# Performance work log

Measured on AMD Instinct MI355X. Metric: run time of the kernel, lower is better.

Reference implementation:

```python
import jax, jax.numpy as jnp
import numpy as np

B, K, N, T, C = 2, 2, 4096, 8, 3
H = 192            # hidden_dim
NODE_DIM = 10
N_LAYERS = 10
KNN = 16           # k nearest neighbours
TOP_FRAC = 0.4
SHARP = 5.0        # mask_sharpness
S = max(int(TOP_FRAC * N), KNN + 1)   # n_select per graph


def _ln(x, g, b, eps=1e-5):
    mu = x.mean(-1, keepdims=True)
    v = ((x - mu) ** 2).mean(-1, keepdims=True)  # biased var, matches nn.LayerNorm
    return (x - mu) / jnp.sqrt(v + eps) * g + b


def setup_inputs() -> dict:
    key = jax.random.key(0)
    ks = jax.random.split(key, 12)
    rn = lambda k, shape: 0.05 * jax.random.normal(k, shape, jnp.float32)
    F0 = 2 * NODE_DIM + 4   # first EdgeConv MLP in-dim
    FR = 2 * H + 4          # remaining EdgeConv MLP in-dim
    L = N_LAYERS - 1
    return {
        "u_base": jax.random.normal(ks[0], (B, K, N, C), jnp.float32),
        "pos": jax.random.uniform(ks[1], (B, N, 3), dtype=jnp.float32),
        "velocity_in": jax.random.normal(ks[2], (B, T, N, C), jnp.float32),
        "airfoil_mask": (jax.random.uniform(ks[3], (B, N)) < 0.05).astype(jnp.float32),
        "conv0_w1": rn(ks[4], (F0, H)), "conv0_b1": jnp.zeros((H,)),
        "conv0_w2": rn(ks[5], (H, H)), "conv0_b2": jnp.zeros((H,)),
        "conv0_g": jnp.ones((H,)), "conv0_be": jnp.zeros((H,)),
        "convs_w1": rn(ks[6], (L, FR, H)), "convs_b1": jnp.zeros((L, H)),
        "convs_w2": rn(ks[7], (L, H, H)), "convs_b2": jnp.zeros((L, H)),
        "convs_g": jnp.ones((L, H)), "convs_be": jnp.zeros((L, H)),
        "head_g": jnp.ones((H,)), "head_be": jnp.zeros((H,)),
        "head_w1": rn(ks[8], (H, H)), "head_b1": jnp.zeros((H,)),
        "head_w2": rn(ks[9], (H, 3)), "head_b2": jnp.zeros((3,)),
    }


def reference(u_base, pos, velocity_in, airfoil_mask,
              conv0_w1, conv0_b1, conv0_w2, conv0_b2, conv0_g, conv0_be,
              convs_w1, convs_b1, convs_w2, convs_b2, convs_g, convs_be,
              head_g, head_be, head_w1, head_b1, head_w2, head_b2):
    # --- variance gating (torch .var/.std are unbiased) ---
    var_pp = jnp.var(velocity_in, axis=1, ddof=1).sum(-1)                      # [B,N]
    var_z = (var_pp - var_pp.mean(1, keepdims=True)) / (
        jnp.std(var_pp, axis=1, ddof=1, keepdims=True) + 1e-8)
    soft_mask = jax.nn.sigmoid(SHARP * var_z) * (1.0 - airfoil_mask)           # [B,N]

    # --- select top-variance points per graph ---
    _, top_idx = jax.lax.top_k(var_pp, S)                                      # [B,S]
    pos_sel = jnp.take_along_axis(pos, top_idx[..., None], axis=1)             # [B,S,3]
    mask_sel = jnp.take_along_axis(soft_mask, top_idx, axis=1)[..., None]      # [B,S,1]
    v_last = velocity_in[:, -1]                                                # [B,N,C]
    ub_sel = jnp.take_along_axis(u_base, top_idx[:, None, :, None], axis=2)    # [B,K,S,C]
    vl_sel = jnp.take_along_axis(v_last, top_idx[..., None], axis=1)           # [B,S,C]
    vf_sel = jnp.take_along_axis(var_pp[..., None], top_idx[..., None], axis=1)
    static = jnp.concatenate([vl_sel, pos_sel, vf_sel], -1)                    # [B,S,7]
    x0 = jnp.concatenate(
        [ub_sel, jnp.broadcast_to(static[:, None], (B, K, S, 7))], -1)         # [B,K,S,10]

    def per_graph(x, pos_b):  # x: [K,S,F0], pos_b: [S,3]
        # kNN graph (self excluded via +inf diagonal, as in the chunked cdist)
        d2 = jnp.sum((pos_b[:, None] - pos_b[None]) ** 2, -1)                  # [S,S]
        d2 = d2.at[jnp.arange(S), jnp.arange(S)].set(jnp.inf)
        _, knn = jax.lax.top_k(-d2, KNN)                                       # [S,KNN]
        # PyG convention with edge_index=stack([targets, sources]):
        # i = edge_index[1] = knn neighbours, j = edge_index[0] = centre nodes
        idx_i = knn.reshape(-1)                     # [E] aggregation targets
        idx_j = jnp.repeat(jnp.arange(S), KNN)      # [E]
        rel = pos_b[idx_i] - pos_b[idx_j]           # pos[edge_index[1]] - pos[edge_index[0]]
        dist = jnp.linalg.norm(rel, axis=-1, keepdims=True)
        ea = jnp.concatenate([rel, dist], -1)       # [E,4]
        ea_b = jnp.broadcast_to(ea, (K,) + ea.shape)

        def conv(h, w1, b1, w2, b2, g, be):
            hi = h[:, idx_i]
            hj = h[:, idx_j]
            m = jnp.concatenate([hi, hj - hi, ea_b], -1)                       # [K,E,2F+4]
            m = jax.nn.gelu(m @ w1 + b1, approximate=False) @ w2 + b2          # [K,E,H]
            agg = jnp.zeros((K, S, H), h.dtype).at[:, idx_i].add(m)
            return _ln(agg, g, be)

        h = conv(x, conv0_w1, conv0_b1, conv0_w2, conv0_b2, conv0_g, conv0_be)
        for l in range(N_LAYERS - 1):
            h = conv(h, convs_w1[l], convs_b1[l], convs_w2[l], convs_b2[l],
                     convs_g[l], convs_be[l]) + h
        hh = _ln(h, head_g, head_be)
        return jax.nn.gelu(hh @ head_w1 + head_b1, approximate=False) @ head_w2 + head_b2

    delta = jax.vmap(per_graph)(x0, pos_sel)        # [B,K,S,3]
    delta = delta * mask_sel[:, None]               # [B,1,S,1]

    def scatter_b(idx, d):  # idx [S], d [K,S,3]
        return jnp.zeros((K, N, C), d.dtype).at[:, idx].set(d)

    delta_full = jax.vmap(scatter_b)(top_idx, delta)            # [B,K,N,C]
    return (u_base + delta_full) * (1.0 - airfoil_mask)[:, None, :, None]
```

## Files before the change

### kernel.cpp

```cpp
#include <hip/hip_runtime.h>
#include <hip/hip_bf16.h>
#include <math.h>

#define B_ 2
#define K_ 2
#define NN_ 4096
#define T_ 8
#define C_ 3
#define H_ 192
#define S_ 1638
#define KK_ 16
#define E_ (S_*KK_)
#define NROW (B_*K_*S_)
#define SHARP_ 5.0f

typedef __hip_bfloat16 bf;
typedef unsigned long long ull;
typedef __bf16 bf16x8 __attribute__((ext_vector_type(8)));
typedef float f32x4 __attribute__((ext_vector_type(4)));

__device__ int   g_isbf16;
__device__ __align__(16) float g_var[B_*NN_];
__device__ __align__(16) float g_vs1[B_*16];
__device__ __align__(16) float g_vs2[B_*16];
__device__ __align__(16) int   g_topidx[B_*S_];
__device__ __align__(16) float g_possel[B_*S_*3];
__device__ __align__(16) float g_masksel[B_*S_];
__device__ __align__(16) float g_x0[NROW*10];
__device__ __align__(16) int   g_knn[B_*E_];
__device__ __align__(16) float g_ea[B_*E_*4];
__device__ __align__(16) int   g_indeg[B_*S_];
__device__ __align__(16) int   g_cursor[B_*S_];
__device__ __align__(16) int   g_off[B_*(S_+1)];
__device__ __align__(16) int   g_list[B_*E_];
__device__ __align__(16) float g_P[(size_t)NROW*H_];
__device__ __align__(16) bf    g_Qbf[(size_t)NROW*H_];
__device__ __align__(16) float g_h[(size_t)NROW*H_];
__device__ __align__(16) bf    g_abf[(size_t)NROW*H_];
__device__ __align__(16) bf    g_w2p[(size_t)11*H_*H_];
__device__ __align__(16) bf    g_wcp[(size_t)9*H_*384];

__device__ __forceinline__ float bf2f(bf x){ return __bfloat162float(x); }
__device__ __forceinline__ float LD(const void* p, long i){
  return g_isbf16 ? __bfloat162float(((const bf*)p)[i]) : ((const float*)p)[i];
}
__device__ __forceinline__ float LDi(const void* p, long i, int isb){
  return isb ? __bfloat162float(((const bf*)p)[i]) : ((const float*)p)[i];
}
__device__ __forceinline__ float gelu_f(float x){
  float ax = fabsf(x)*0.70710678118654752f;
  float t = 1.0f/(1.0f + 0.3275911f*ax);
  float p = t*(0.254829592f + t*(-0.284496736f + t*(1.421413741f + t*(-1.453152027f + t*1.061405429f))));
  float er = 1.0f - p*__expf(-ax*ax);
  er = copysignf(er, x);
  return 0.5f*x*(1.0f + er);
}

__global__ __launch_bounds__(256) void k_var(const void* __restrict__ vel,
                                             const void* __restrict__ ub,
                                             const void* __restrict__ pos){
  __shared__ int s_bad;
  int b = blockIdx.y;
  int bx = blockIdx.x;
  int tid = threadIdx.x;
  if (tid == 0) s_bad = 0;
  __syncthreads();
  {
    const bf* pa = (const bf*)ub; const bf* pb = (const bf*)pos; const bf* pc = (const bf*)vel;
    int bad = 0;
    #pragma unroll
    for (int s = 0; s < 2; ++s){
      float va = __bfloat162float(pa[tid + s*256]);
      float vb = __bfloat162float(pb[tid + s*256]);
      float vc = __bfloat162float(pc[tid + s*256]);
      if (!(fabsf(va) <= 1000.f)) bad = 1;
      if (!(fabsf(vb) <= 1000.f)) bad = 1;
      if (!(fabsf(vc) <= 1000.f)) bad = 1;
    }
    if (bad) atomicOr(&s_bad, 1);
  }
  __syncthreads();
  int isb = (s_bad == 0) ? 1 : 0;
  if (bx == 0 && b == 0 && tid == 0) g_isbf16 = isb;
  int zi = (b*16 + bx)*256 + tid;
  if (zi < B_*S_){ g_indeg[zi] = 0; g_cursor[zi] = 0; }
  int n = bx*256 + tid;
  float v = 0.f;
  #pragma unroll
  for (int c = 0; c < 3; ++c){
    float x[8];
    #pragma unroll
    for (int t = 0; t < 8; ++t)
      x[t] = LDi(vel, ((long)(b*T_+t)*NN_ + n)*3 + c, isb);
    float m = __fadd_rn(__fadd_rn(__fadd_rn(x[0],x[1]), __fadd_rn(x[2],x[3])),
                        __fadd_rn(__fadd_rn(x[4],x[5]), __fadd_rn(x[6],x[7]))) / 8.0f;
    float d[8];
    #pragma unroll
    for (int t = 0; t < 8; ++t){ float dd = __fadd_rn(x[t], -m); d[t] = __fmul_rn(dd,dd); }
    float sv = __fadd_rn(__fadd_rn(__fadd_rn(d[0],d[1]), __fadd_rn(d[2],d[3])),
                         __fadd_rn(__fadd_rn(d[4],d[5]), __fadd_rn(d[6],d[7])));
    v = __fadd_rn(v, sv / 7.0f);
  }
  g_var[b*NN_ + n] = v;
  float s1 = v, s2 = v*v;
  #pragma unroll
  for (int o = 32; o; o >>= 1){ s1 += __shfl_xor(s1,o,64); s2 += __shfl_xor(s2,o,64); }
  __shared__ float r1[4], r2[4];
  int lane = tid & 63, wid = tid >> 6;
  if (!lane){ r1[wid]=s1; r2[wid]=s2; }
  __syncthreads();
  if (tid == 0){
    g_vs1[b*16 + bx] = r1[0]+r1[1]+r1[2]+r1[3];
    g_vs2[b*16 + bx] = r2[0]+r2[1]+r2[2]+r2[3];
  }
}

__global__ __launch_bounds__(256) void k_rank(const void* __restrict__ pos){
  int b = blockIdx.y;
  int i = blockIdx.x*4 + (threadIdx.x >> 6);
  int lane = threadIdx.x & 63;
  float vi = g_var[b*NN_+i];
  int rank = 0;
  for (int j = lane; j < NN_; j += 64){
    float vj = g_var[b*NN_+j];
    rank += ((vj > vi) || (vj == vi && j < i)) ? 1 : 0;
  }
  #pragma unroll
  for (int o = 32; o; o >>= 1) rank += __shfl_xor(rank, o, 64);
  if (lane == 0 && rank < S_){
    g_topidx[b*S_ + rank] = i;
    long gi = (long)(b*S_ + rank)*3;
    g_possel[gi+0] = LD(pos, ((long)b*NN_+i)*3+0);
    g_possel[gi+1] = LD(pos, ((long)b*NN_+i)*3+1);
    g_possel[gi+2] = LD(pos, ((long)b*NN_+i)*3+2);
  }
}

#define GATH_BLKS 7
__global__ __launch_bounds__(256) void k_knngather(const void* __restrict__ pos,
                                                   const void* __restrict__ ub,
                                                   const void* __restrict__ vel,
                                                   const void* __restrict__ air){
  int b = blockIdx.y;
  int bx = blockIdx.x;
  if (bx < GATH_BLKS){
    int s = bx*256 + threadIdx.x;
    if (s >= S_) return;
    int gi = b*S_ + s;
    int node = g_topidx[gi];
    float px = g_possel[(long)gi*3+0];
    float py = g_possel[(long)gi*3+1];
    float pz = g_possel[(long)gi*3+2];
    float S1 = 0.f, S2 = 0.f;
    #pragma unroll
    for (int t = 0; t < 16; ++t){ S1 += g_vs1[b*16+t]; S2 += g_vs2[b*16+t]; }
    float mean = S1*(1.f/NN_);
    float sd = sqrtf(fmaxf((S2 - S1*S1*(1.f/NN_))*(1.f/(NN_-1)), 0.f));
    float vf = g_var[b*NN_+node];
    float z = (vf-mean)/(sd+1e-8f);
    float sig = 1.f/(1.f+expf(-SHARP_*z));
    g_masksel[gi] = sig*(1.f - LD(air, b*NN_+node));
    float vl0 = LD(vel, ((long)(b*T_+7)*NN_+node)*3+0);
    float vl1 = LD(vel, ((long)(b*T_+7)*NN_+node)*3+1);
    float vl2 = LD(vel, ((long)(b*T_+7)*NN_+node)*3+2);
    for (int k = 0; k < K_; ++k){
      long row = (long)(b*K_+k)*S_ + s;
      float* x = g_x0 + row*10;
      x[0]=LD(ub, ((long)(b*K_+k)*NN_+node)*3+0);
      x[1]=LD(ub, ((long)(b*K_+k)*NN_+node)*3+1);
      x[2]=LD(ub, ((long)(b*K_+k)*NN_+node)*3+2);
      x[3]=vl0; x[4]=vl1; x[5]=vl2;
      x[6]=px;  x[7]=py;  x[8]=pz;
      x[9]=vf;
    }
    return;
  }
  __shared__ float px[S_], py[S_], pz[S_];
  int j = (bx - GATH_BLKS)*4 + (threadIdx.x >> 6);
  int lane = threadIdx.x & 63;
  for (int t = threadIdx.x; t < S_; t += 256){
    long gi = (long)(b*S_ + t)*3;
    px[t] = g_possel[gi+0];
    py[t] = g_possel[gi+1];
    pz[t] = g_possel[gi+2];
  }
  __syncthreads();
  if (j >= S_) return;
  float xj=px[j], yj=py[j], zj=pz[j];
  float dist[KK_]; int id[KK_];
  #pragma unroll
  for (int t = 0; t < KK_; ++t){ dist[t]=3.0e38f; id[t]=0x7fffffff; }
  for (int c = lane; c < S_; c += 64){
    if (c == j) continue;
    float dx=__fadd_rn(px[c],-xj), dy=__fadd_rn(py[c],-yj), dz=__fadd_rn(pz[c],-zj);
    float d2 = __fadd_rn(__fadd_rn(__fmul_rn(dx,dx), __fmul_rn(dy,dy)), __fmul_rn(dz,dz));
    if (d2 < dist[KK_-1]){
      int p = 0;
      #pragma unroll
      for (int q = 0; q < KK_; ++q) p += (dist[q] <= d2) ? 1 : 0;
      #pragma unroll
      for (int q = KK_-1; q >= 1; --q){
        bool mv = (q > p);
        dist[q] = mv ? dist[q-1] : dist[q];
        id[q]   = mv ? id[q-1]   : id[q];
      }
      #pragma unroll
      for (int q = 0; q < KK_; ++q){ if (q == p){ dist[q] = d2; id[q] = c; } }
    }
  }
  unsigned selid = 0;
  #pragma unroll
  for (int t = 0; t < KK_; ++t){
    float mv = dist[0];
    #pragma unroll
    for (int o = 32; o; o >>= 1) mv = fminf(mv, __shfl_xor(mv, o, 64));
    unsigned cand = (dist[0] == mv) ? (unsigned)id[0] : 0xFFFFFFFFu;
    #pragma unroll
    for (int o = 32; o; o >>= 1){
      unsigned other = (unsigned)__shfl_xor((int)cand, o, 64);
      cand = (cand < other) ? cand : other;
    }
    if (dist[0] == mv && (unsigned)id[0] == cand){
      #pragma unroll
      for (int q = 0; q < KK_-1; ++q){ dist[q]=dist[q+1]; id[q]=id[q+1]; }
      dist[KK_-1] = 3.0e38f; id[KK_-1] = 0x7fffffff;
    }
    if (lane == t) selid = cand;
  }
  if (lane < KK_){
    int i = (int)selid;
    g_knn[(b*S_+j)*KK_ + lane] = i;
    float rx = __fadd_rn(px[i],-xj), ry = __fadd_rn(py[i],-yj), rz = __fadd_rn(pz[i],-zj);
    float dd = sqrtf(__fadd_rn(__fadd_rn(__fmul_rn(rx,rx), __fmul_rn(ry,ry)), __fmul_rn(rz,rz)));
    float* o = g_ea + ((long)b*E_ + j*KK_ + lane)*4;
    o[0]=rx; o[1]=ry; o[2]=rz; o[3]=dd;
    atomicAdd(&g_indeg[b*S_+i], 1);
  }
}

__global__ void k_scan(){
  __shared__ int sA[2048], sB[2048];
  int b = blockIdx.x, tid = threadIdx.x;
  for (int i = tid; i < 2048; i += 1024) sA[i] = (i < S_) ? g_indeg[b*S_+i] : 0;
  __syncthreads();
  int *src = sA, *dst = sB;
  for (int d = 1; d < 2048; d <<= 1){
    for (int i = tid; i < 2048; i += 1024) dst[i] = src[i] + (i >= d ? src[i-d] : 0);
    __syncthreads();
    int* t2 = src; src = dst; dst = t2;
  }
  if (tid == 0) g_off[b*(S_+1)] = 0;
  for (int i = tid; i < S_; i += 1024) g_off[b*(S_+1)+i+1] = src[i];
}

#define PW2_BLKS 1584
#define PWC_BLKS 2592
#define INIT_BLKS 192
#define FILL_BLKS 205
#define PROJ_BLKS 410
__global__ void k_packall(const void* __restrict__ c0w2, const void* __restrict__ cw2,
                          const void* __restrict__ hw1, const void* __restrict__ cw1,
                          const void* __restrict__ ub, const void* __restrict__ air,
                          float* __restrict__ out, const void* __restrict__ c0w1){
  int blk = blockIdx.x;
  if (blk < PW2_BLKS){
    int gi = blk*256 + threadIdx.x;
    if (gi >= 11*H_*H_) return;
    int mat = gi / (H_*H_), r = gi - mat*(H_*H_);
    int k = r / H_, n = r - (r/H_)*H_;
    float v;
    if (mat == 0)      v = LD(c0w2, (long)k*H_ + n);
    else if (mat <= 9) v = LD(cw2, (long)(mat-1)*H_*H_ + (long)k*H_ + n);
    else               v = LD(hw1, (long)k*H_ + n);
    int t = k>>5, q = (k>>3)&3, jj = k&7;
    g_w2p[(size_t)mat*H_*H_ + (((t*4+q)*H_ + n)*8 + jj)] = __float2bfloat16(v);
  } else if (blk < PW2_BLKS + PWC_BLKS){
    int gi = (blk - PW2_BLKS)*256 + threadIdx.x;
    if (gi >= 9*H_*384) return;
    int l = gi / (H_*384), r = gi - l*(H_*384);
    int k = r / 384, n = r - (r/384)*384;
    long base = (long)l*388*H_;
    float v;
    if (n < H_) v = LD(cw1, base + (long)k*H_ + n) - LD(cw1, base + (long)(H_+k)*H_ + n);
    else        v = LD(cw1, base + (long)(H_+k)*H_ + (n-H_));
    int t = k>>5, q = (k>>3)&3, jj = k&7;
    g_wcp[(size_t)l*(H_*384) + (((t*4+q)*384 + n)*8 + jj)] = __float2bfloat16(v);
  } else if (blk < PW2_BLKS + PWC_BLKS + INIT_BLKS){
    int gi = (blk - PW2_BLKS - PWC_BLKS)*256 + threadIdx.x;
    int n = (gi/3) % NN_;
    int b = gi / (K_*NN_*C_);
    float a = 1.f - LD(air, b*NN_+n);
    out[gi] = LD(ub, gi) * a;
  } else if (blk < PW2_BLKS + PWC_BLKS + INIT_BLKS + FILL_BLKS){
    int idx = (blk - PW2_BLKS - PWC_BLKS - INIT_BLKS)*256 + threadIdx.x;
    if (idx >= B_*E_) return;
    int b = idx / E_, e = idx - b*E_;
    int i = g_knn[idx];
    int slot = atomicAdd(&g_cursor[b*S_+i], 1);
    g_list[b*E_ + g_off[b*(S_+1)+i] + slot] = e;
  } else {
    __shared__ float xs[16][10];
    __shared__ float wP[10][192];
    __shared__ float wQ[10][192];
    int tid = threadIdx.x;
    long rowBase = (long)(blk - PW2_BLKS - PWC_BLKS - INIT_BLKS - FILL_BLKS) * 16;
    for (int idx = tid; idx < 1920; idx += 256){
      int f = idx / 192, n = idx - (idx/192)*192;
      float a = LD(c0w1, f*H_+n), b = LD(c0w1, (10+f)*H_+n);
      wP[f][n] = a - b; wQ[f][n] = b;
    }
    for (int idx = tid; idx < 160; idx += 256){
      int r = idx / 10, f = idx - (idx/10)*10;
      long row = rowBase + r; if (row >= NROW) row = NROW-1;
      xs[r][f] = g_x0[row*10 + f];
    }
    __syncthreads();
    for (int o = tid; o < 16*384; o += 256){
      int r = o / 384, n = o - (o/384)*384;
      long row = rowBase + r;
      if (row >= NROW) continue;
      float acc = 0.f;
      if (n < 192){
        #pragma unroll
        for (int f = 0; f < 10; ++f) acc += xs[r][f]*wP[f][n];
        g_P[row*192 + n] = acc;
      } else {
        int nc = n - 192;
        #pragma unroll
        for (int f = 0; f < 10; ++f) acc += xs[r][f]*wQ[f][nc];
        g_Qbf[row*192 + nc] = __float2bfloat16(acc);
      }
    }
  }
}

__global__ __launch_bounds__(192) void k_aggedge(const void* __restrict__ w1cB, long w1cO,
                                                 const void* __restrict__ b1B, long b1O){
  int o = blockIdx.x;
  int t = o & 7, s = o >> 3;
  int bk = t >> 1;
  int row = bk*S_ + 2*s + (t & 1);
  int col = threadIdx.x;
  int i = row - bk*S_, b = bk >> 1;
  int off = g_off[b*(S_+1)+i];
  int deg = g_off[b*(S_+1)+i+1] - off;
  float w0 = LD(w1cB, w1cO+col),       w1v = LD(w1cB, w1cO+H_+col);
  float w2v = LD(w1cB, w1cO+2*H_+col), w3v = LD(w1cB, w1cO+3*H_+col);
  float base = g_P[(size_t)row*H_ + col] + LD(b1B, b1O+col);
  const int* lst = g_list + b*E_ + off;
  const bf* Q = g_Qbf + (size_t)bk*S_*H_;
  const float* EA = g_ea + (size_t)b*E_*4;
  float acc = 0.f;
  int d = 0;
  for (; d + 8 <= deg; d += 8){
    int e[8];
    #pragma unroll
    for (int u = 0; u < 8; ++u) e[u] = lst[d+u];
    float4 a[8];
    #pragma unroll
    for (int u = 0; u < 8; ++u) a[u] = *reinterpret_cast<const float4*>(EA + (size_t)e[u]*4);
    float qv[8];
    #pragma unroll
    for (int u = 0; u < 8; ++u) qv[u] = bf2f(Q[(size_t)(e[u]>>4)*H_ + col]);
    #pragma unroll
    for (int u = 0; u < 8; ++u)
      acc += gelu_f(base + qv[u] + a[u].x*w0 + a[u].y*w1v + a[u].z*w2v + a[u].w*w3v);
  }
  for (; d + 4 <= deg; d += 4){
    int e0 = lst[d], e1 = lst[d+1], e2 = lst[d+2], e3 = lst[d+3];
    float4 a0 = *reinterpret_cast<const float4*>(EA + (size_t)e0*4);
    float4 a1 = *reinterpret_cast<const float4*>(EA + (size_t)e1*4);
    float4 a2 = *reinterpret_cast<const float4*>(EA + (size_t)e2*4);
    float4 a3 = *reinterpret_cast<const float4*>(EA + (size_t)e3*4);
    float q0 = bf2f(Q[(size_t)(e0>>4)*H_ + col]);
    float q1 = bf2f(Q[(size_t)(e1>>4)*H_ + col]);
    float q2 = bf2f(Q[(size_t)(e2>>4)*H_ + col]);
    float q3 = bf2f(Q[(size_t)(e3>>4)*H_ + col]);
    acc += gelu_f(base + q0 + a0.x*w0 + a0.y*w1v + a0.z*w2v + a0.w*w3v);
    acc += gelu_f(base + q1 + a1.x*w0 + a1.y*w1v + a1.z*w2v + a1.w*w3v);
    acc += gelu_f(base + q2 + a2.x*w0 + a2.y*w1v + a2.z*w2v + a2.w*w3v);
    acc += gelu_f(base + q3 + a3.x*w0 + a3.y*w1v + a3.z*w2v + a3.w*w3v);
  }
  for (; d < deg; ++d){
    int e = lst[d];
    float4 a = *reinterpret_cast<const float4*>(EA + (size_t)e*4);
    float qv = bf2f(Q[(size_t)(e>>4)*H_ + col]);
    acc += gelu_f(base + qv + a.x*w0 + a.y*w1v + a.z*w2v + a.w*w3v);
  }
  g_abf[(size_t)row*H_ + col] = __float2bfloat16(acc);
}

template<int RES, int DOPQ, int DOHEAD>
__global__ __launch_bounds__(512) void k_lnpq(const void* __restrict__ biasB, long biasO,
                                              const void* __restrict__ gB, long gO,
                                              const void* __restrict__ beB, long beO,
                                              int bOff, int pqOff,
                                              const void* __restrict__ hg, const void* __restrict__ hbe,
                                              const void* __restrict__ hb1, const void* __restrict__ hw2,
                                              const void* __restrict__ hb2, const void* __restrict__ ubase,
                                              const void* __restrict__ air, float* __restrict__ out,
                                              int M){
  const bf* A  = g_abf;
  const bf* Bp = g_w2p + bOff;
  int tid = threadIdx.x;
  int wv = tid >> 6, lane = tid & 63;
  int q = lane >> 4, l16 = lane & 15;
  long rowBase = (long)blockIdx.x * 16;
  __shared__ float tile[16][200];
  __shared__ bf    ybf[16][200];
  __shared__ float srow[16], rrow[16];
  {
    f32x4 acc[2];
    acc[0] = (f32x4){0.f,0.f,0.f,0.f};
    acc[1] = (f32x4){0.f,0.f,0.f,0.f};
    #pragma unroll
    for (int t = 0; t < 6; ++t){
      int kof = t*32 + q*8;
      long r = rowBase + l16; if (r >= M) r = M-1;
      bf16x8 af = *reinterpret_cast<const bf16x8*>(A + r*192 + kof);
      #pragma unroll
      for (int jj = 0; jj < 2; ++jj){
        int j = wv + jj*8;
        if (j < 12){
          int n = j*16 + l16;
          bf16x8 bfr = *reinterpret_cast<const bf16x8*>(Bp + (((t*4+q)*192 + n)*8));
          acc[jj] = __builtin_amdgcn_mfma_f32_16x16x32_bf16(af, bfr, acc[jj], 0,0,0);
        }
      }
    }
    float degf[4];
    #pragma unroll
    for (int r = 0; r < 4; ++r){
      int lr = q*4 + r;
      long row = rowBase + lr;
      long rowc = (row < M) ? row : (M-1);
      int bk = (int)(rowc / S_); int i = (int)(rowc - (long)bk*S_); int b = bk >> 1;
      degf[r] = (float)(g_off[b*(S_+1)+i+1] - g_off[b*(S_+1)+i]);
    }
    #pragma unroll
    for (int jj = 0; jj < 2; ++jj){
      int j = wv + jj*8;
      if (j < 12){
        int col = j*16 + l16;
        float bb = LD(biasB, biasO + col);
        #pragma unroll
        for (int r = 0; r < 4; ++r){
          int lr = q*4 + r;
          tile[lr][col] = acc[jj][r] + degf[r]*bb;
        }
      }
    }
  }
  __syncthreads();
  {
    int lr = wv*2 + (lane >> 5);
    int k32 = lane & 31;
    float s = 0.f, qq = 0.f;
    #pragma unroll
    for (int c6 = 0; c6 < 6; ++c6){ float x = tile[lr][k32 + c6*32]; s += x; qq += x*x; }
    #pragma unroll
    for (int o = 1; o < 32; o <<= 1){ s += __shfl_xor(s,o,64); qq += __shfl_xor(qq,o,64); }
    if (k32 == 0){
      float mu = s*(1.f/H_);
      float var = qq*(1.f/H_) - mu*mu;
      srow[lr] = mu;
      rrow[lr] = rsqrtf(fmaxf(var, 0.f) + 1e-5f);
    }
  }
  __syncthreads();
  for (int o = tid; o < 16*192; o += 512){
    int lr = o / 192, col = o - (o/192)*192;
    long row = rowBase + lr;
    long rowc = (row < M) ? row : (M-1);
    float y = (tile[lr][col] - srow[lr])*rrow[lr]*LD(gB,gO+col) + LD(beB,beO+col);
    if (RES) y += g_h[rowc*192 + col];
    if (!DOHEAD){
      if (row < M) g_h[row*192 + col] = y;
      ybf[lr][col] = __float2bfloat16(y);
    } else {
      tile[lr][col] = y;
    }
  }
  if (DOPQ){
    __syncthreads();
    const bf* Bq = g_wcp + pqOff;
    f32x4 acc2[3];
    #pragma unroll
    for (int jj = 0; jj < 3; ++jj) acc2[jj] = (f32x4){0.f,0.f,0.f,0.f};
    #pragma unroll
    for (int t = 0; t < 6; ++t){
      int kof = t*32 + q*8;
      bf16x8 af = *reinterpret_cast<const bf16x8*>(&ybf[l16][kof]);
      #pragma unroll
      for (int jj = 0; jj < 3; ++jj){
        int n = (wv*3 + jj)*16 + l16;
        bf16x8 bfr = *reinterpret_cast<const bf16x8*>(Bq + (((t*4+q)*384 + n)*8));
        acc2[jj] = __builtin_amdgcn_mfma_f32_16x16x32_bf16(af, bfr, acc2[jj], 0,0,0);
      }
    }
    #pragma unroll
    for (int jj = 0; jj < 3; ++jj){
      int col = (wv*3 + jj)*16 + l16;
      #pragma unroll
      for (int r = 0; r < 4; ++r){
        long row = rowBase + q*4 + r;
        if (row < M){
          float v = acc2[jj][r];
          if (col < 192) g_P[row*192 + col] = v;
          else           g_Qbf[row*192 + (col-192)] = __float2bfloat16(v);
        }
      }
    }
  }
  if (DOHEAD){
    __syncthreads();
    {
      int lr = wv*2 + (lane >> 5);
      int k32 = lane & 31;
      float s = 0.f, qq = 0.f;
      #pragma unroll
      for (int c6 = 0; c6 < 6; ++c6){ float x = tile[lr][k32 + c6*32]; s += x; qq += x*x; }
      #pragma unroll
      for (int o = 1; o < 32; o <<= 1){ s += __shfl_xor(s,o,64); qq += __shfl_xor(qq,o,64); }
      if (k32 == 0){
        float mu = s*(1.f/H_);
        float var = qq*(1.f/H_) - mu*mu;
        srow[lr] = mu;
        rrow[lr] = rsqrtf(fmaxf(var, 0.f) + 1e-5f);
      }
    }
    __syncthreads();
    for (int o = tid; o < 16*192; o += 512){
      int lr = o / 192, col = o - (o/192)*192;
      ybf[lr][col] = __float2bfloat16((tile[lr][col] - srow[lr])*rrow[lr]*LD(hg,col) + LD(hbe,col));
    }
    __syncthreads();
    {
      const bf* Bh = g_w2p + 10*H_*H_;
      f32x4 hacc[2];
      hacc[0] = (f32x4){0.f,0.f,0.f,0.f};
      hacc[1] = (f32x4){0.f,0.f,0.f,0.f};
      #pragma unroll
      for (int t = 0; t < 6; ++t){
        int kof = t*32 + q*8;
        bf16x8 af = *reinterpret_cast<const bf16x8*>(&ybf[l16][kof]);
        #pragma unroll
        for (int jj = 0; jj < 2; ++jj){
          int j = wv + jj*8;
          if (j < 12){
            int n = j*16 + l16;
            bf16x8 bfr = *reinterpret_cast<const bf16x8*>(Bh + (((t*4+q)*192 + n)*8));
            hacc[jj] = __builtin_amdgcn_mfma_f32_16x16x32_bf16(af, bfr, hacc[jj], 0,0,0);
          }
        }
      }
      #pragma unroll
      for (int jj = 0; jj < 2; ++jj){
        int j = wv + jj*8;
        if (j < 12){
          int col = j*16 + l16;
          float bb = LD(hb1, col);
          #pragma unroll
          for (int r = 0; r < 4; ++r){
            int lr = q*4 + r;
            tile[lr][col] = gelu_f(hacc[jj][r] + bb);
          }
        }
      }
    }
    __syncthreads();
    {
      int lr = wv*2 + (lane >> 5);
      int k32 = lane & 31;
      float p0 = 0.f, p1 = 0.f, p2 = 0.f;
      #pragma unroll
      for (int c6 = 0; c6 < 6; ++c6){
        int col = k32 + c6*32;
        float tv = tile[lr][col];
        p0 += tv*LD(hw2, col*3+0);
        p1 += tv*LD(hw2, col*3+1);
        p2 += tv*LD(hw2, col*3+2);
      }
      #pragma unroll
      for (int o = 1; o < 32; o <<= 1){
        p0 += __shfl_xor(p0,o,64);
        p1 += __shfl_xor(p1,o,64);
        p2 += __shfl_xor(p2,o,64);
      }
      if (k32 == 0){
        long row = rowBase + lr;
        if (row < M){
          int bk = (int)(row / S_), s = (int)(row - (long)bk*S_), b = bk >> 1;
          float msk = g_masksel[b*S_+s];
          int node = g_topidx[b*S_+s];
          float am = 1.f - LD(air, b*NN_+node);
          float d0 = p0 + LD(hb2,0), d1 = p1 + LD(hb2,1), d2 = p2 + LD(hb2,2);
          long oi = ((long)bk*NN_ + node)*3;
          out[oi+0] = (LD(ubase, oi+0) + d0*msk)*am;
          out[oi+1] = (LD(ubase, oi+1) + d1*msk)*am;
          out[oi+2] = (LD(ubase, oi+2) + d2*msk)*am;
        }
      }
    }
  }
}

extern "C" void kernel_launch(void* const* d_in, const int* in_sizes, int n_in,
                              void* d_out, int out_size, void* d_ws, size_t ws_size,
                              hipStream_t stream) {
  (void)in_sizes; (void)n_in; (void)d_ws; (void)ws_size; (void)out_size;
  const void* u_base = d_in[0];
  const void* pos    = d_in[1];
  const void* vel    = d_in[2];
  const void* air    = d_in[3];
  const void* c0w1   = d_in[4];
  const void* c0b1   = d_in[5];
  const void* c0w2   = d_in[6];
  const void* c0b2   = d_in[7];
  const void* c0g    = d_in[8];
  const void* c0be   = d_in[9];
  const void* cw1    = d_in[10];
  const void* cb1    = d_in[11];
  const void* cw2    = d_in[12];
  const void* cb2    = d_in[13];
  const void* cg     = d_in[14];
  const void* cbe    = d_in[15];
  const void* hg     = d_in[16];
  const void* hbe    = d_in[17];
  const void* hw1    = d_in[18];
  const void* hb1    = d_in[19];
  const void* hw2    = d_in[20];
  const void* hb2    = d_in[21];
  float* out = (float*)d_out;

  k_var<<<dim3(16, B_), 256, 0, stream>>>(vel, u_base, pos);
  k_rank<<<dim3(NN_/4, B_), 256, 0, stream>>>(pos);
  k_knngather<<<dim3(GATH_BLKS + (S_+3)/4, B_), 256, 0, stream>>>(pos, u_base, vel, air);
  k_scan<<<B_, 1024, 0, stream>>>();
  k_packall<<<PW2_BLKS + PWC_BLKS + INIT_BLKS + FILL_BLKS + PROJ_BLKS, 256, 0, stream>>>(
      c0w2, cw2, hw1, cw1, u_base, air, out, c0w1);

  const int GN16 = (NROW + 15) / 16;
  for (int l = 0; l < 10; ++l){
    long w1cO = (l == 0) ? 20L*H_ : ((long)(l-1)*388 + 384)*H_;
    const void* w1cB = (l == 0) ? c0w1 : cw1;
    long lOff = (l == 0) ? 0 : (long)(l-1)*H_;
    const void* b1B = (l == 0) ? c0b1 : cb1;
    k_aggedge<<<NROW, 192, 0, stream>>>(w1cB, w1cO, b1B, lOff);

    const void* b2B = (l == 0) ? c0b2 : cb2;
    const void* gB  = (l == 0) ? c0g  : cg;
    const void* beB = (l == 0) ? c0be : cbe;
    if (l == 0)
      k_lnpq<0,1,0><<<GN16, 512, 0, stream>>>(b2B, lOff, gB, lOff, beB, lOff, 0,        0,
                                              hg, hbe, hb1, hw2, hb2, u_base, air, out, NROW);
    else if (l < 9)
      k_lnpq<1,1,0><<<GN16, 512, 0, stream>>>(b2B, lOff, gB, lOff, beB, lOff, l*H_*H_, l*H_*384,
                                              hg, hbe, hb1, hw2, hb2, u_base, air, out, NROW);
    else
      k_lnpq<1,0,1><<<GN16, 512, 0, stream>>>(b2B, lOff, gB, lOff, beB, lOff, l*H_*H_, 0,
                                              hg, hbe, hb1, hw2, hb2, u_base, air, out, NROW);
  }
}
```

Baseline: 547.4 us.

## Fuse edge aggregation and LayerNorm/projection into one per-layer kernel with tile flags

```diff
diff --git a/kernel.cpp b/kernel.cpp
--- a/kernel.cpp
+++ b/kernel.cpp
@@ -13,6 +13,8 @@
 #define E_ (S_*KK_)
 #define NROW (B_*K_*S_)
 #define SHARP_ 5.0f
+#define NT_ 410
+#define NAGG_BLKS 3280
 
 typedef __hip_bfloat16 bf;
 typedef unsigned long long ull;
@@ -34,11 +36,12 @@
 __device__ __align__(16) int   g_off[B_*(S_+1)];
 __device__ __align__(16) int   g_list[B_*E_];
 __device__ __align__(16) float g_P[(size_t)NROW*H_];
-__device__ __align__(16) bf    g_Qbf[(size_t)NROW*H_];
+__device__ __align__(16) bf    g_Qbf[2*(size_t)NROW*H_];
 __device__ __align__(16) float g_h[(size_t)NROW*H_];
 __device__ __align__(16) bf    g_abf[(size_t)NROW*H_];
 __device__ __align__(16) bf    g_w2p[(size_t)11*H_*H_];
 __device__ __align__(16) bf    g_wcp[(size_t)9*H_*384];
+__device__ __align__(16) int   g_tdone[10*NT_];
 
 __device__ __forceinline__ float bf2f(bf x){ return __bfloat162float(x); }
 __device__ __forceinline__ float LD(const void* p, long i){
@@ -84,6 +87,7 @@
   if (bx == 0 && b == 0 && tid == 0) g_isbf16 = isb;
   int zi = (b*16 + bx)*256 + tid;
   if (zi < B_*S_){ g_indeg[zi] = 0; g_cursor[zi] = 0; }
+  if (zi < 10*NT_) g_tdone[zi] = 0;
   int n = bx*256 + tid;
   float v = 0.f;
   #pragma unroll
@@ -334,78 +338,100 @@
   }
 }
 
-__global__ __launch_bounds__(192) void k_aggedge(const void* __restrict__ w1cB, long w1cO,
-                                                 const void* __restrict__ b1B, long b1O){
-  int o = blockIdx.x;
-  int t = o & 7, s = o >> 3;
-  int bk = t >> 1;
-  int row = bk*S_ + 2*s + (t & 1);
-  int col = threadIdx.x;
-  int i = row - bk*S_, b = bk >> 1;
-  int off = g_off[b*(S_+1)+i];
-  int deg = g_off[b*(S_+1)+i+1] - off;
-  float w0 = LD(w1cB, w1cO+col),       w1v = LD(w1cB, w1cO+H_+col);
-  float w2v = LD(w1cB, w1cO+2*H_+col), w3v = LD(w1cB, w1cO+3*H_+col);
-  float base = g_P[(size_t)row*H_ + col] + LD(b1B, b1O+col);
-  const int* lst = g_list + b*E_ + off;
-  const bf* Q = g_Qbf + (size_t)bk*S_*H_;
-  const float* EA = g_ea + (size_t)b*E_*4;
-  float acc = 0.f;
-  int d = 0;
-  for (; d + 8 <= deg; d += 8){
-    int e[8];
-    #pragma unroll
-    for (int u = 0; u < 8; ++u) e[u] = lst[d+u];
-    float4 a[8];
-    #pragma unroll
-    for (int u = 0; u < 8; ++u) a[u] = *reinterpret_cast<const float4*>(EA + (size_t)e[u]*4);
-    float qv[8];
-    #pragma unroll
-    for (int u = 0; u < 8; ++u) qv[u] = bf2f(Q[(size_t)(e[u]>>4)*H_ + col]);
-    #pragma unroll
-    for (int u = 0; u < 8; ++u)
-      acc += gelu_f(base + qv[u] + a[u].x*w0 + a[u].y*w1v + a[u].z*w2v + a[u].w*w3v);
-  }
-  for (; d + 4 <= deg; d += 4){
-    int e0 = lst[d], e1 = lst[d+1], e2 = lst[d+2], e3 = lst[d+3];
-    float4 a0 = *reinterpret_cast<const float4*>(EA + (size_t)e0*4);
-    float4 a1 = *reinterpret_cast<const float4*>(EA + (size_t)e1*4);
-    float4 a2 = *reinterpret_cast<const float4*>(EA + (size_t)e2*4);
-    float4 a3 = *reinterpret_cast<const float4*>(EA + (size_t)e3*4);
-    float q0 = bf2f(Q[(size_t)(e0>>4)*H_ + col]);
-    float q1 = bf2f(Q[(size_t)(e1>>4)*H_ + col]);
-    float q2 = bf2f(Q[(size_t)(e2>>4)*H_ + col]);
-    float q3 = bf2f(Q[(size_t)(e3>>4)*H_ + col]);
-    acc += gelu_f(base + q0 + a0.x*w0 + a0.y*w1v + a0.z*w2v + a0.w*w3v);
-    acc += gelu_f(base + q1 + a1.x*w0 + a1.y*w1v + a1.z*w2v + a1.w*w3v);
-    acc += gelu_f(base + q2 + a2.x*w0 + a2.y*w1v + a2.z*w2v + a2.w*w3v);
-    acc += gelu_f(base + q3 + a3.x*w0 + a3.y*w1v + a3.z*w2v + a3.w*w3v);
-  }
-  for (; d < deg; ++d){
-    int e = lst[d];
-    float4 a = *reinterpret_cast<const float4*>(EA + (size_t)e*4);
-    float qv = bf2f(Q[(size_t)(e>>4)*H_ + col]);
-    acc += gelu_f(base + qv + a.x*w0 + a.y*w1v + a.z*w2v + a.w*w3v);
-  }
-  g_abf[(size_t)row*H_ + col] = __float2bfloat16(acc);
-}
-
 template<int RES, int DOPQ, int DOHEAD>
-__global__ __launch_bounds__(512) void k_lnpq(const void* __restrict__ biasB, long biasO,
-                                              const void* __restrict__ gB, long gO,
-                                              const void* __restrict__ beB, long beO,
-                                              int bOff, int pqOff,
-                                              const void* __restrict__ hg, const void* __restrict__ hbe,
-                                              const void* __restrict__ hb1, const void* __restrict__ hw2,
-                                              const void* __restrict__ hb2, const void* __restrict__ ubase,
-                                              const void* __restrict__ air, float* __restrict__ out,
-                                              int M){
+__global__ __launch_bounds__(512) void k_layer(
+    int layer, int qcur, int qnxt,
+    const void* __restrict__ w1cB, long w1cO,
+    const void* __restrict__ b1B, long b1O,
+    const void* __restrict__ biasB, long biasO,
+    const void* __restrict__ gB, long gO,
+    const void* __restrict__ beB, long beO,
+    int bOff, int pqOff,
+    const void* __restrict__ hg, const void* __restrict__ hbe,
+    const void* __restrict__ hb1, const void* __restrict__ hw2,
+    const void* __restrict__ hb2, const void* __restrict__ ubase,
+    const void* __restrict__ air, float* __restrict__ out,
+    int M){
+  int tid = threadIdx.x;
+  if (blockIdx.x < NAGG_BLKS){
+    int o = blockIdx.x;
+    int t = o & 7, s = o >> 3;
+    int bk = t >> 1;
+    int jp = 2*s + (t & 1);
+    if (jp >= 819) return;
+    int tile = (bk*S_ + 2*jp) >> 4;
+    int sub = tid / 192;
+    if (sub < 2){
+      int col = tid - sub*192;
+      int i = 2*jp + sub;
+      int row = bk*S_ + i;
+      int b = bk >> 1;
+      int off = g_off[b*(S_+1)+i];
+      int deg = g_off[b*(S_+1)+i+1] - off;
+      float w0 = LD(w1cB, w1cO+col),       w1v = LD(w1cB, w1cO+H_+col);
+      float w2v = LD(w1cB, w1cO+2*H_+col), w3v = LD(w1cB, w1cO+3*H_+col);
+      float base = g_P[(size_t)row*H_ + col] + LD(b1B, b1O+col);
+      const int* lst = g_list + b*E_ + off;
+      const bf* Q = g_Qbf + (size_t)qcur*NROW*H_ + (size_t)bk*S_*H_;
+      const float* EA = g_ea + (size_t)b*E_*4;
+      float acc = 0.f;
+      int d = 0;
+      for (; d + 8 <= deg; d += 8){
+        int e[8];
+        #pragma unroll
+        for (int u = 0; u < 8; ++u) e[u] = lst[d+u];
+        float4 a[8];
+        #pragma unroll
+        for (int u = 0; u < 8; ++u) a[u] = *reinterpret_cast<const float4*>(EA + (size_t)e[u]*4);
+        float qv[8];
+        #pragma unroll
+        for (int u = 0; u < 8; ++u) qv[u] = bf2f(Q[(size_t)(e[u]>>4)*H_ + col]);
+        #pragma unroll
+        for (int u = 0; u < 8; ++u)
+          acc += gelu_f(base + qv[u] + a[u].x*w0 + a[u].y*w1v + a[u].z*w2v + a[u].w*w3v);
+      }
+      for (; d + 4 <= deg; d += 4){
+        int e0 = lst[d], e1 = lst[d+1], e2 = lst[d+2], e3 = lst[d+3];
+        float4 a0 = *reinterpret_cast<const float4*>(EA + (size_t)e0*4);
+        float4 a1 = *reinterpret_cast<const float4*>(EA + (size_t)e1*4);
+        float4 a2 = *reinterpret_cast<const float4*>(EA + (size_t)e2*4);
+        float4 a3 = *reinterpret_cast<const float4*>(EA + (size_t)e3*4);
+        float q0 = bf2f(Q[(size_t)(e0>>4)*H_ + col]);
+        float q1 = bf2f(Q[(size_t)(e1>>4)*H_ + col]);
+        float q2 = bf2f(Q[(size_t)(e2>>4)*H_ + col]);
+        float q3 = bf2f(Q[(size_t)(e3>>4)*H_ + col]);
+        acc += gelu_f(base + q0 + a0.x*w0 + a0.y*w1v + a0.z*w2v + a0.w*w3v);
+        acc += gelu_f(base + q1 + a1.x*w0 + a1.y*w1v + a1.z*w2v + a1.w*w3v);
+        acc += gelu_f(base + q2 + a2.x*w0 + a2.y*w1v + a2.z*w2v + a2.w*w3v);
+        acc += gelu_f(base + q3 + a3.x*w0 + a3.y*w1v + a3.z*w2v + a3.w*w3v);
+      }
+      for (; d < deg; ++d){
+        int e = lst[d];
+        float4 a = *reinterpret_cast<const float4*>(EA + (size_t)e*4);
+        float qv = bf2f(Q[(size_t)(e>>4)*H_ + col]);
+        acc += gelu_f(base + qv + a.x*w0 + a.y*w1v + a.z*w2v + a.w*w3v);
+      }
+      g_abf[(size_t)row*H_ + col] = __float2bfloat16(acc);
+    }
+    __syncthreads();
+    if (tid == 0)
+      __hip_atomic_fetch_add(&g_tdone[layer*NT_ + tile], 2,
+                             __ATOMIC_RELEASE, __HIP_MEMORY_SCOPE_AGENT);
+    return;
+  }
+  int tileIdx = blockIdx.x - NAGG_BLKS;
+  if (tid == 0){
+    int need = (tileIdx == NT_-1) ? 8 : 16;
+    while (__hip_atomic_load(&g_tdone[layer*NT_ + tileIdx],
+                             __ATOMIC_ACQUIRE, __HIP_MEMORY_SCOPE_AGENT) < need)
+      __builtin_amdgcn_s_sleep(16);
+  }
+  __syncthreads();
   const bf* A  = g_abf;
   const bf* Bp = g_w2p + bOff;
-  int tid = threadIdx.x;
   int wv = tid >> 6, lane = tid & 63;
   int q = lane >> 4, l16 = lane & 15;
-  long rowBase = (long)blockIdx.x * 16;
+  long rowBase = (long)tileIdx * 16;
   __shared__ float tile[16][200];
   __shared__ bf    ybf[16][200];
   __shared__ float srow[16], rrow[16];
@@ -484,6 +510,7 @@
   if (DOPQ){
     __syncthreads();
     const bf* Bq = g_wcp + pqOff;
+    bf* Qout = g_Qbf + (size_t)qnxt*NROW*H_;
     f32x4 acc2[3];
     #pragma unroll
     for (int jj = 0; jj < 3; ++jj) acc2[jj] = (f32x4){0.f,0.f,0.f,0.f};
@@ -507,7 +534,7 @@
         if (row < M){
           float v = acc2[jj][r];
           if (col < 192) g_P[row*192 + col] = v;
-          else           g_Qbf[row*192 + (col-192)] = __float2bfloat16(v);
+          else           Qout[row*192 + (col-192)] = __float2bfloat16(v);
         }
       }
     }
@@ -640,25 +667,27 @@
   k_packall<<<PW2_BLKS + PWC_BLKS + INIT_BLKS + FILL_BLKS + PROJ_BLKS, 256, 0, stream>>>(
       c0w2, cw2, hw1, cw1, u_base, air, out, c0w1);
 
-  const int GN16 = (NROW + 15) / 16;
+  const int GRID = NAGG_BLKS + NT_;
   for (int l = 0; l < 10; ++l){
     long w1cO = (l == 0) ? 20L*H_ : ((long)(l-1)*388 + 384)*H_;
     const void* w1cB = (l == 0) ? c0w1 : cw1;
     long lOff = (l == 0) ? 0 : (long)(l-1)*H_;
     const void* b1B = (l == 0) ? c0b1 : cb1;
-    k_aggedge<<<NROW, 192, 0, stream>>>(w1cB, w1cO, b1B, lOff);
-
     const void* b2B = (l == 0) ? c0b2 : cb2;
     const void* gB  = (l == 0) ? c0g  : cg;
     const void* beB = (l == 0) ? c0be : cbe;
+    int qcur = l & 1, qnxt = (l+1) & 1;
     if (l == 0)
-      k_lnpq<0,1,0><<<GN16, 512, 0, stream>>>(b2B, lOff, gB, lOff, beB, lOff, 0,        0,
-                                              hg, hbe, hb1, hw2, hb2, u_base, air, out, NROW);
+      k_layer<0,1,0><<<GRID, 512, 0, stream>>>(l, qcur, qnxt, w1cB, w1cO, b1B, lOff,
+                                               b2B, lOff, gB, lOff, beB, lOff, 0, 0,
+                                               hg, hbe, hb1, hw2, hb2, u_base, air, out, NROW);
     else if (l < 9)
-      k_lnpq<1,1,0><<<GN16, 512, 0, stream>>>(b2B, lOff, gB, lOff, beB, lOff, l*H_*H_, l*H_*384,
-                                              hg, hbe, hb1, hw2, hb2, u_base, air, out, NROW);
+      k_layer<1,1,0><<<GRID, 512, 0, stream>>>(l, qcur, qnxt, w1cB, w1cO, b1B, lOff,
+                                               b2B, lOff, gB, lOff, beB, lOff, l*H_*H_, l*H_*384,
+                                               hg, hbe, hb1, hw2, hb2, u_base, air, out, NROW);
     else
-      k_lnpq<1,0,1><<<GN16, 512, 0, stream>>>(b2B, lOff, gB, lOff, beB, lOff, l*H_*H_, 0,
-                                              hg, hbe, hb1, hw2, hb2, u_base, air, out, NROW);
-  }
-}
+      k_layer<1,0,1><<<GRID, 512, 0, stream>>>(l, qcur, qnxt, w1cB, w1cO, b1B, lOff,
+                                               b2B, lOff, gB, lOff, beB, lOff, l*H_*H_, 0,
+                                               hg, hbe, hb1, hw2, hb2, u_base, air, out, NROW);
+  }
+}
```

New measurement: 1.183 ms. +116.2%, slower.
